# Kernel optimization log

Hardware: AMD Instinct MI355X
Metric: run time of the kernel (lower is better)

## Reference

```python
import jax, jax.numpy as jnp
import numpy as np

B, S, D = 2, 1024, 2048
L = 4
HQ, HKV, HD = 32, 8, 64
I = 5632
V = 32000
EPS = 1e-5
THETA = 10000.0
SCALE = HD ** -0.5
GROUP = HQ // HKV


def setup_inputs() -> dict:
    key = jax.random.key(0)
    ks = jax.random.split(key, 8)
    s = 0.02
    return {
        "input_ids": jax.random.randint(ks[0], (B, S), 0, V, dtype=jnp.int32),
        "positions": jnp.broadcast_to(jnp.arange(S, dtype=jnp.int32), (B, S)),
        "embed": jax.random.normal(ks[1], (V, D), jnp.float32) * s,
        "w_qkv": jax.random.normal(ks[2], (L, D, (HQ + 2 * HKV) * HD), jnp.float32) * s,
        "w_o": jax.random.normal(ks[3], (L, HQ * HD, D), jnp.float32) * s,
        "w_gate_up": jax.random.normal(ks[4], (L, D, 2 * I), jnp.float32) * s,
        "w_down": jax.random.normal(ks[5], (L, I, D), jnp.float32) * s,
        "ln1_w": jnp.ones((L, D), jnp.float32),
        "ln2_w": jnp.ones((L, D), jnp.float32),
        "norm_w": jnp.ones((D,), jnp.float32),
    }


def rmsnorm(x, w):
    var = jnp.mean(x * x, axis=-1, keepdims=True)
    return x * jax.lax.rsqrt(var + EPS) * w


def rope(positions, x):
    # x: [B, S, H, HD]; neox-style rotate-half RoPE
    inv_freq = 1.0 / (THETA ** (jnp.arange(0, HD, 2, dtype=jnp.float32) / HD))
    ang = positions.astype(jnp.float32)[..., None] * inv_freq  # [B, S, HD/2]
    cos = jnp.cos(ang)[:, :, None, :]
    sin = jnp.sin(ang)[:, :, None, :]
    x1, x2 = jnp.split(x, 2, axis=-1)
    return jnp.concatenate([x1 * cos - x2 * sin, x2 * cos + x1 * sin], axis=-1)


def llama_forward(input_ids, positions, embed, w_qkv, w_o, w_gate_up, w_down,
                  ln1_w, ln2_w, norm_w):
    h = embed[input_ids]                      # [B, S, D]
    res = jnp.zeros_like(h)
    causal = jnp.tril(jnp.ones((S, S), dtype=bool))
    neg = jnp.asarray(jnp.finfo(h.dtype).min, h.dtype)

    def layer(carry, params):
        h, res = carry
        wqkv, wo, wgu, wd, l1, l2 = params
        # fused RMSNorm + residual-add (vllm RMSNorm(x, residual) semantics)
        res = h + res
        h = rmsnorm(res, l1)
        # QKV projection + RoPE
        qkv = h @ wqkv
        q, k, v = jnp.split(qkv, [HQ * HD, (HQ + HKV) * HD], axis=-1)
        q = q.reshape(B, S, HQ, HD)
        k = k.reshape(B, S, HKV, HD)
        v = v.reshape(B, S, HKV, HD)
        q = rope(positions, q)
        k = rope(positions, k)
        # GQA: broadcast kv heads across query groups
        k = jnp.repeat(k, GROUP, axis=2)      # [B, S, HQ, HD]
        v = jnp.repeat(v, GROUP, axis=2)
        scores = jnp.einsum('bqhd,bkhd->bhqk', q, k) * SCALE
        scores = jnp.where(causal, scores, neg)
        attn = jax.nn.softmax(scores, axis=-1)
        o = jnp.einsum('bhqk,bkhd->bqhd', attn, v).reshape(B, S, HQ * HD)
        h = o @ wo
        # post-attention fused RMSNorm + residual
        res = h + res
        h = rmsnorm(res, l2)
        # SwiGLU MLP
        gu = h @ wgu
        g, u = jnp.split(gu, 2, axis=-1)
        h = (jax.nn.silu(g) * u) @ wd
        return (h, res), None

    (h, res), _ = jax.lax.scan(layer, (h, res),
                               (w_qkv, w_o, w_gate_up, w_down, ln1_w, ln2_w))
    return rmsnorm(h + res, norm_w)


def reference(input_ids, positions, embed, w_qkv, w_o, w_gate_up, w_down,
              ln1_w, ln2_w, norm_w):
    return llama_forward(input_ids, positions, embed, w_qkv, w_o, w_gate_up,
                         w_down, ln1_w, ln2_w, norm_w)
```

## Files before the change

### kernel.cpp

```cpp
#include <hip/hip_runtime.h>
#include <hip/hip_bf16.h>

#define B_ 2
#define S_ 1024
#define T_ (B_*S_)
#define D_ 2048
#define L_ 4
#define HQ_ 32
#define HKV_ 8
#define HD_ 64
#define I_ 5632
#define EPS_ 1e-5f
#define SCALE_ 0.125f

typedef __attribute__((ext_vector_type(4))) float  float4v;
typedef __attribute__((ext_vector_type(8))) short  short8v;
typedef __attribute__((ext_vector_type(4))) short  short4v;

#define GLOAD16(g, l) \
  __builtin_amdgcn_global_load_lds((const __attribute__((address_space(1))) void*)(g), \
                                   (__attribute__((address_space(3))) void*)(l), 16, 0, 0)

__device__ __forceinline__ short f2bf(float f) {
  union { float f; unsigned u; } c; c.f = f;
  unsigned u = c.u + 0x7fffu + ((c.u >> 16) & 1u);
  return (short)(u >> 16);
}

__device__ __forceinline__ void xcd_swizzle(int gx, int gy, int& bx, int& by) {
  int nwg = gx * gy;
  int orig = by * gx + bx;
  int q = nwg >> 3, r = nwg & 7;
  int xcd = orig & 7, loc = orig >> 3;
  int swz = (xcd < r ? xcd * (q + 1) : r * (q + 1) + (xcd - r) * q) + loc;
  bx = swz / gy;
  by = swz - bx * gy;
}

__global__ __launch_bounds__(256)
void transpose_layer(const float* __restrict__ wq, const float* __restrict__ wo,
                     const float* __restrict__ wg, const float* __restrict__ wd,
                     short* __restrict__ tq, short* __restrict__ to_,
                     short* __restrict__ tg, short* __restrict__ td) {
  int id = blockIdx.x;
  const float* in; short* out; int K, N, bxt, byt;
  if (id < 1536)      { in = wq; out = tq;
                        K = 2048; N = 3072;  bxt = id % 48;  byt = id / 48; }
  else if (id < 2560) { id -= 1536; in = wo; out = to_;
                        K = 2048; N = 2048;  bxt = id % 32;  byt = id / 32; }
  else if (id < 8192) { id -= 2560; in = wg; out = tg;
                        K = 2048; N = 11264; bxt = id % 176; byt = id / 176; }
  else                { id -= 8192; in = wd; out = td;
                        K = 5632; N = 2048;  bxt = id % 32;  byt = id / 32; }
  __shared__ float t[64][65];
  const int bx = bxt * 64;
  const int by = byt * 64;
  const int tid = threadIdx.x;
  const int lr = tid >> 4;
  const int lc = (tid & 15) * 4;
  #pragma unroll
  for (int j = 0; j < 64; j += 16) {
    float4v v = *(const float4v*)(in + (size_t)(by + lr + j) * N + bx + lc);
    t[lr + j][lc] = v[0]; t[lr + j][lc + 1] = v[1];
    t[lr + j][lc + 2] = v[2]; t[lr + j][lc + 3] = v[3];
  }
  __syncthreads();
  const int nr = tid >> 3;
  const int kc = (tid & 7) * 8;
  #pragma unroll
  for (int j = 0; j < 64; j += 32) {
    short8v y;
    #pragma unroll
    for (int e = 0; e < 8; e++) y[e] = f2bf(t[kc + e][nr + j]);
    *(short8v*)(out + (size_t)(bx + nr + j) * K + by + kc) = y;
  }
}

__global__ __launch_bounds__(256)
void embed_gather(const int* __restrict__ ids, const float* __restrict__ embed,
                  float* __restrict__ h) {
  size_t i = (size_t)blockIdx.x * 256 + threadIdx.x;
  int t  = (int)(i >> 9);
  int d4 = (int)(i & 511);
  ((float4v*)h)[i] = ((const float4v*)(embed + (size_t)ids[t] * D_))[d4];
}

__global__ __launch_bounds__(256)
void rmsnorm_kernel(const float* __restrict__ x, float* __restrict__ res,
                    const float* __restrict__ w, void* __restrict__ outp,
                    int first, int bf16out) {
  const int row = blockIdx.x;
  const int tid = threadIdx.x;
  const size_t base = (size_t)row * D_;
  float4v v0, v1;
  if (first) {
    v0 = ((const float4v*)(x + base))[tid * 2];
    v1 = ((const float4v*)(x + base))[tid * 2 + 1];
    ((float4v*)(res + base))[tid * 2]     = v0;
    ((float4v*)(res + base))[tid * 2 + 1] = v1;
  } else {
    v0 = ((const float4v*)(res + base))[tid * 2];
    v1 = ((const float4v*)(res + base))[tid * 2 + 1];
  }
  float ss = v0[0]*v0[0] + v0[1]*v0[1] + v0[2]*v0[2] + v0[3]*v0[3]
           + v1[0]*v1[0] + v1[1]*v1[1] + v1[2]*v1[2] + v1[3]*v1[3];
  #pragma unroll
  for (int off = 32; off > 0; off >>= 1) ss += __shfl_xor(ss, off, 64);
  __shared__ float red[4];
  if ((tid & 63) == 0) red[tid >> 6] = ss;
  __syncthreads();
  float tot = red[0] + red[1] + red[2] + red[3];
  float rs = rsqrtf(tot * (1.0f / D_) + EPS_);
  float4v w0 = ((const float4v*)w)[tid * 2];
  float4v w1 = ((const float4v*)w)[tid * 2 + 1];
  float4v o0 = v0 * rs * w0;
  float4v o1 = v1 * rs * w1;
  if (bf16out) {
    short8v y;
    #pragma unroll
    for (int k = 0; k < 4; k++) { y[k] = f2bf(o0[k]); y[k + 4] = f2bf(o1[k]); }
    ((short8v*)((char*)outp + base * 2))[tid] = y;
  } else {
    float* op = (float*)outp + base;
    ((float4v*)op)[tid * 2]     = o0;
    ((float4v*)op)[tid * 2 + 1] = o1;
  }
}

__global__ __launch_bounds__(512, 4)
void gemm_big128(const short* __restrict__ A, const short* __restrict__ Bt,
                 float* __restrict__ C, int M, int N, int K, int addto) {
  __shared__ short sA[2][128 * 64];
  __shared__ short sB[2][128 * 64];
  int bx = blockIdx.x, by = blockIdx.y;
  xcd_swizzle(gridDim.x, gridDim.y, bx, by);
  const int tid  = threadIdx.x;
  const int lane = tid & 63;
  const int wv   = tid >> 6;
  const int wr   = wv >> 2;
  const int wc   = wv & 3;
  const int row0 = by * 128;
  const int col0 = bx * 128;
  const int fr = lane & 15;
  const int g  = lane >> 4;
  const int NT = K >> 6;

  float4v acc[4][2] = {};

  int rS[2], cS[2];
  #pragma unroll
  for (int k = 0; k < 2; k++) {
    int s = tid + k * 512;
    rS[k] = s >> 3;
    cS[k] = (((s & 7) ^ (rS[k] & 7)) << 3);
  }

#define STAGE128(t, buf) do { \
    int k0_ = (t) << 6; \
    _Pragma("unroll") \
    for (int k_ = 0; k_ < 2; k_++) \
      GLOAD16(A  + (size_t)(row0 + rS[k_]) * K + k0_ + cS[k_], \
              &sA[buf][(tid + k_ * 512) * 8]); \
    _Pragma("unroll") \
    for (int k_ = 0; k_ < 2; k_++) \
      GLOAD16(Bt + (size_t)(col0 + rS[k_]) * K + k0_ + cS[k_], \
              &sB[buf][(tid + k_ * 512) * 8]); \
  } while (0)

  STAGE128(0, 0);

  for (int t = 0; t < NT; t++) {
    const int cur = t & 1;
    if (t + 1 < NT) {
      STAGE128(t + 1, cur ^ 1);
      asm volatile("s_waitcnt vmcnt(4)" ::: "memory");
    } else {
      asm volatile("s_waitcnt vmcnt(0)" ::: "memory");
    }
    __builtin_amdgcn_s_barrier();
    __builtin_amdgcn_sched_barrier(0);

    const short* pA = &sA[cur][(wr * 64) * 64];
    const short* pB = &sB[cur][(wc * 32) * 64];
    #pragma unroll
    for (int ks = 0; ks < 2; ks++) {
      const int fswk = ((((ks << 2) | g) ^ (fr & 7)) << 3);
      short8v bfr[2], afr[4];
      #pragma unroll
      for (int ni = 0; ni < 2; ni++)
        bfr[ni] = *(const short8v*)(pB + (ni * 16 + fr) * 64 + fswk);
      #pragma unroll
      for (int m4 = 0; m4 < 4; m4++)
        afr[m4] = *(const short8v*)(pA + (m4 * 16 + fr) * 64 + fswk);
      __builtin_amdgcn_s_setprio(1);
      #pragma unroll
      for (int m4 = 0; m4 < 4; m4++)
        #pragma unroll
        for (int ni = 0; ni < 2; ni++)
          acc[m4][ni] = __builtin_amdgcn_mfma_f32_16x16x32_bf16(
              afr[m4], bfr[ni], acc[m4][ni], 0, 0, 0);
      __builtin_amdgcn_s_setprio(0);
    }
    asm volatile("" ::: "memory");
    __builtin_amdgcn_s_barrier();
  }

  #pragma unroll
  for (int m4 = 0; m4 < 4; m4++)
    #pragma unroll
    for (int ni = 0; ni < 2; ni++) {
      size_t base = (size_t)(row0 + wr * 64 + m4 * 16 + g * 4) * N
                    + col0 + wc * 32 + ni * 16 + fr;
      if (addto) {
        #pragma unroll
        for (int r = 0; r < 4; r++)
          C[base + (size_t)r * N] += acc[m4][ni][r];
      } else {
        #pragma unroll
        for (int r = 0; r < 4; r++)
          C[base + (size_t)r * N] = acc[m4][ni][r];
      }
    }
#undef STAGE128
}

__global__ __launch_bounds__(512, 2)
void gemm_glu_big(const short* __restrict__ A, const short* __restrict__ Bt,
                  short* __restrict__ mlp, int K) {
  __shared__ short sA[2][128 * 64];
  __shared__ short sG[2][128 * 64];
  __shared__ short sU[2][128 * 64];
  int bx = blockIdx.x, by = blockIdx.y;
  xcd_swizzle(gridDim.x, gridDim.y, bx, by);
  const int tid  = threadIdx.x;
  const int lane = tid & 63;
  const int wv   = tid >> 6;
  const int wr   = wv >> 2;
  const int wc   = wv & 3;
  const int row0 = by * 128;
  const int col0 = bx * 128;
  const int fr = lane & 15;
  const int g  = lane >> 4;
  const int NT = K >> 6;

  float4v accg[4][2] = {};
  float4v accu[4][2] = {};

  int rS[2], cS[2];
  #pragma unroll
  for (int k = 0; k < 2; k++) {
    int s = tid + k * 512;
    rS[k] = s >> 3;
    cS[k] = (((s & 7) ^ (rS[k] & 7)) << 3);
  }

#define STAGEGLU(t, buf) do { \
    int k0_ = (t) << 6; \
    _Pragma("unroll") \
    for (int k_ = 0; k_ < 2; k_++) \
      GLOAD16(A  + (size_t)(row0 + rS[k_]) * K + k0_ + cS[k_], \
              &sA[buf][(tid + k_ * 512) * 8]); \
    _Pragma("unroll") \
    for (int k_ = 0; k_ < 2; k_++) \
      GLOAD16(Bt + (size_t)(col0 + rS[k_]) * K + k0_ + cS[k_], \
              &sG[buf][(tid + k_ * 512) * 8]); \
    _Pragma("unroll") \
    for (int k_ = 0; k_ < 2; k_++) \
      GLOAD16(Bt + (size_t)(col0 + I_ + rS[k_]) * K + k0_ + cS[k_], \
              &sU[buf][(tid + k_ * 512) * 8]); \
  } while (0)

  STAGEGLU(0, 0);

  for (int t = 0; t < NT; t++) {
    const int cur = t & 1;
    if (t + 1 < NT) {
      STAGEGLU(t + 1, cur ^ 1);
      asm volatile("s_waitcnt vmcnt(6)" ::: "memory");
    } else {
      asm volatile("s_waitcnt vmcnt(0)" ::: "memory");
    }
    __builtin_amdgcn_s_barrier();
    __builtin_amdgcn_sched_barrier(0);

    const short* pA = &sA[cur][(wr * 64) * 64];
    const short* pG = &sG[cur][(wc * 32) * 64];
    const short* pU = &sU[cur][(wc * 32) * 64];
    #pragma unroll
    for (int ks = 0; ks < 2; ks++) {
      const int fswk = ((((ks << 2) | g) ^ (fr & 7)) << 3);
      short8v bg[2], bu[2], afr[4];
      #pragma unroll
      for (int ni = 0; ni < 2; ni++) {
        bg[ni] = *(const short8v*)(pG + (ni * 16 + fr) * 64 + fswk);
        bu[ni] = *(const short8v*)(pU + (ni * 16 + fr) * 64 + fswk);
      }
      #pragma unroll
      for (int m4 = 0; m4 < 4; m4++)
        afr[m4] = *(const short8v*)(pA + (m4 * 16 + fr) * 64 + fswk);
      __builtin_amdgcn_s_setprio(1);
      #pragma unroll
      for (int m4 = 0; m4 < 4; m4++)
        #pragma unroll
        for (int ni = 0; ni < 2; ni++) {
          accg[m4][ni] = __builtin_amdgcn_mfma_f32_16x16x32_bf16(
              afr[m4], bg[ni], accg[m4][ni], 0, 0, 0);
          accu[m4][ni] = __builtin_amdgcn_mfma_f32_16x16x32_bf16(
              afr[m4], bu[ni], accu[m4][ni], 0, 0, 0);
        }
      __builtin_amdgcn_s_setprio(0);
    }
    asm volatile("" ::: "memory");
    __builtin_amdgcn_s_barrier();
  }

  #pragma unroll
  for (int m4 = 0; m4 < 4; m4++)
    #pragma unroll
    for (int ni = 0; ni < 2; ni++) {
      size_t base = (size_t)(row0 + wr * 64 + m4 * 16 + g * 4) * I_
                    + col0 + wc * 32 + ni * 16 + fr;
      #pragma unroll
      for (int r = 0; r < 4; r++) {
        float gv = accg[m4][ni][r], uv = accu[m4][ni][r];
        mlp[base + (size_t)r * I_] = f2bf(gv / (1.0f + __expf(-gv)) * uv);
      }
    }
#undef STAGEGLU
}

__global__ __launch_bounds__(512, 4)
void gemm_qkv_big(const short* __restrict__ A, const short* __restrict__ Bt,
                  const float* __restrict__ tab, short* __restrict__ qbf,
                  short* __restrict__ kbf, short* __restrict__ vtbf, int K) {
  __shared__ short sA[2][128 * 64];
  __shared__ short sB[2][128 * 64];
  int bx = blockIdx.x, by = blockIdx.y;
  xcd_swizzle(gridDim.x, gridDim.y, bx, by);
  const int tid  = threadIdx.x;
  const int lane = tid & 63;
  const int wv   = tid >> 6;
  const int wm   = (wv >> 1) * 32;
  const int wn   = (wv & 1) * 64;
  const int row0 = by * 128;
  const int col0 = bx * 128;
  const int fr = lane & 15;
  const int g  = lane >> 4;
  const int NT = K >> 6;

  float4v acc[2][4] = {};

  int rS[2], cS[2];
  #pragma unroll
  for (int k = 0; k < 2; k++) {
    int s = tid + k * 512;
    rS[k] = s >> 3;
    cS[k] = (((s & 7) ^ (rS[k] & 7)) << 3);
  }

#define STAGEQKV(t, buf) do { \
    int k0_ = (t) << 6; \
    _Pragma("unroll") \
    for (int k_ = 0; k_ < 2; k_++) \
      GLOAD16(A  + (size_t)(row0 + rS[k_]) * K + k0_ + cS[k_], \
              &sA[buf][(tid + k_ * 512) * 8]); \
    _Pragma("unroll") \
    for (int k_ = 0; k_ < 2; k_++) \
      GLOAD16(Bt + (size_t)(col0 + rS[k_]) * K + k0_ + cS[k_], \
              &sB[buf][(tid + k_ * 512) * 8]); \
  } while (0)

  STAGEQKV(0, 0);

  for (int t = 0; t < NT; t++) {
    const int cur = t & 1;
    if (t + 1 < NT) {
      STAGEQKV(t + 1, cur ^ 1);
      asm volatile("s_waitcnt vmcnt(4)" ::: "memory");
    } else {
      asm volatile("s_waitcnt vmcnt(0)" ::: "memory");
    }
    __builtin_amdgcn_s_barrier();
    __builtin_amdgcn_sched_barrier(0);

    const short* pA = &sA[cur][wm * 64];
    const short* pB = &sB[cur][wn * 64];
    #pragma unroll
    for (int ks = 0; ks < 2; ks++) {
      const int fswk = ((((ks << 2) | g) ^ (fr & 7)) << 3);
      short8v afr[2], bfr[4];
      #pragma unroll
      for (int m2 = 0; m2 < 2; m2++)
        afr[m2] = *(const short8v*)(pA + (m2 * 16 + fr) * 64 + fswk);
      #pragma unroll
      for (int ni = 0; ni < 4; ni++)
        bfr[ni] = *(const short8v*)(pB + (ni * 16 + fr) * 64 + fswk);
      __builtin_amdgcn_s_setprio(1);
      #pragma unroll
      for (int m2 = 0; m2 < 2; m2++)
        #pragma unroll
        for (int ni = 0; ni < 4; ni++)
          acc[m2][ni] = __builtin_amdgcn_mfma_f32_16x16x32_bf16(
              afr[m2], bfr[ni], acc[m2][ni], 0, 0, 0);
      __builtin_amdgcn_s_setprio(0);
    }
    asm volatile("" ::: "memory");
    __builtin_amdgcn_s_barrier();
  }

  const int head = (col0 + wn) >> 6;
  if (head < HQ_ + HKV_) {
    const float sc = (head < HQ_) ? SCALE_ : 1.0f;
    short* dst = (head < HQ_) ? qbf : kbf;
    const int hh = (head < HQ_) ? head : head - HQ_;
    const int HN = (head < HQ_) ? HQ_ : HKV_;
    #pragma unroll
    for (int m2 = 0; m2 < 2; m2++)
      #pragma unroll
      for (int jj = 0; jj < 2; jj++)
        #pragma unroll
        for (int r = 0; r < 4; r++) {
          int m = row0 + wm + m2 * 16 + g * 4 + r;
          int b = m >> 10, s = m & (S_ - 1);
          int d1 = jj * 16 + fr;
          float x1 = acc[m2][jj][r], x2 = acc[m2][jj + 2][r];
          const float* tb = tab + (size_t)m * 64 + d1 * 2;
          float c = tb[0], sn = tb[1];
          size_t base = ((size_t)((b * HN + hh) * S_ + s)) * HD_;
          dst[base + d1]      = f2bf((x1 * c - x2 * sn) * sc);
          dst[base + d1 + 32] = f2bf((x2 * c + x1 * sn) * sc);
        }
  } else {
    const int vh = head - HQ_ - HKV_;
    #pragma unroll
    for (int m2 = 0; m2 < 2; m2++) {
      int m0 = row0 + wm + m2 * 16 + g * 4;
      int b = m0 >> 10, s0 = m0 & (S_ - 1);
      #pragma unroll
      for (int ni = 0; ni < 4; ni++) {
        int d = ni * 16 + fr;
        short4v w;
        #pragma unroll
        for (int r = 0; r < 4; r++) w[r] = f2bf(acc[m2][ni][r]);
        *(short4v*)(&vtbf[((size_t)((b * HKV_ + vh) * HD_ + d)) * S_ + s0]) = w;
      }
    }
  }
#undef STAGEQKV
}

__global__ __launch_bounds__(256)
void rope_table(const int* __restrict__ pos, float* __restrict__ tab) {
  int i = blockIdx.x * 256 + threadIdx.x;
  int t = i >> 5, ii = i & 31;
  float p = (float)pos[t];
  float freq = __expf(-(float)ii * (9.210340371976184f / 32.0f));
  float ang = p * freq;
  tab[2 * i]     = cosf(ang);
  tab[2 * i + 1] = sinf(ang);
}

#define KPAD 68

__global__ __launch_bounds__(512)
void attn_mfma(const short* __restrict__ qbf, const short* __restrict__ kbf,
               const short* __restrict__ vtbf, short* __restrict__ obf) {
  __shared__ short sK[64 * KPAD];
  __shared__ short sVt[64 * KPAD];
  __shared__ short sP[8][16 * KPAD];
  const int qb = blockIdx.x;
  const int h  = blockIdx.y;
  const int b  = blockIdx.z;
  const int kh = h >> 2;
  const int tid  = threadIdx.x;
  const int lane = tid & 63;
  const int wv   = tid >> 6;
  const int q0 = qb * 128;
  const int cc = lane & 15;
  const int g  = lane >> 4;

  short8v qf0, qf1;
  {
    const short* qrow = qbf + ((size_t)((b * HQ_ + h) * S_ + q0 + wv * 16 + cc)) * HD_;
    qf0 = *(const short8v*)(qrow + g * 8);
    qf1 = *(const short8v*)(qrow + g * 8 + 32);
  }
  float4v accO[4] = {};
  float m_r[4], l_r[4];
  #pragma unroll
  for (int r = 0; r < 4; r++) { m_r[r] = -1e30f; l_r[r] = 0.f; }

  const short* kb = kbf  + ((size_t)(b * HKV_ + kh)) * S_ * HD_;
  const short* vb = vtbf + ((size_t)(b * HKV_ + kh)) * HD_ * S_;

  const int rr = tid >> 3;
  const int ch = (tid & 7) * 8;

  short8v kr = *(const short8v*)(kb + (size_t)rr * HD_ + ch);
  short8v vr = *(const short8v*)(vb + (size_t)rr * S_ + ch);

  const int nb = 2 * qb + 1;
  for (int jt = 0; jt <= nb; jt++) {
    const int j0 = jt * 64;
    __syncthreads();
    *(short8v*)(&sK[rr * KPAD + ch])  = kr;
    *(short8v*)(&sVt[rr * KPAD + ch]) = vr;
    __syncthreads();

    if (jt < nb) {
      const int j0n = j0 + 64;
      kr = *(const short8v*)(kb + (size_t)(j0n + rr) * HD_ + ch);
      vr = *(const short8v*)(vb + (size_t)rr * S_ + j0n + ch);
    }

    float4v sc[4] = {};
    #pragma unroll
    for (int ct = 0; ct < 4; ct++) {
      short8v k0 = *(const short8v*)(&sK[(ct * 16 + cc) * KPAD + g * 8]);
      short8v k1 = *(const short8v*)(&sK[(ct * 16 + cc) * KPAD + g * 8 + 32]);
      __builtin_amdgcn_s_setprio(1);
      sc[ct] = __builtin_amdgcn_mfma_f32_16x16x32_bf16(qf0, k0, sc[ct], 0, 0, 0);
      sc[ct] = __builtin_amdgcn_mfma_f32_16x16x32_bf16(qf1, k1, sc[ct], 0, 0, 0);
      __builtin_amdgcn_s_setprio(0);
    }
    if (jt >= 2 * qb) {
      #pragma unroll
      for (int ct = 0; ct < 4; ct++)
        #pragma unroll
        for (int r = 0; r < 4; r++)
          if (j0 + ct * 16 + cc > q0 + wv * 16 + g * 4 + r) sc[ct][r] = -1e30f;
    }
    float pmv[4], dmax = -1e30f;
    #pragma unroll
    for (int r = 0; r < 4; r++) {
      float pm = fmaxf(fmaxf(sc[0][r], sc[1][r]), fmaxf(sc[2][r], sc[3][r]));
      pm = fmaxf(pm, __shfl_xor(pm, 1, 64));
      pm = fmaxf(pm, __shfl_xor(pm, 2, 64));
      pm = fmaxf(pm, __shfl_xor(pm, 4, 64));
      pm = fmaxf(pm, __shfl_xor(pm, 8, 64));
      pmv[r] = pm;
      dmax = fmaxf(dmax, pm - m_r[r]);
    }
    if (!__all(dmax <= 8.0f)) {
      float corr[4];
      #pragma unroll
      for (int r = 0; r < 4; r++) {
        float mn = fmaxf(m_r[r], pmv[r]);
        corr[r] = __expf(m_r[r] - mn);
        m_r[r] = mn;
        l_r[r] *= corr[r];
      }
      #pragma unroll
      for (int dt = 0; dt < 4; dt++)
        #pragma unroll
        for (int r = 0; r < 4; r++)
          accO[dt][r] *= corr[r];
    }
    #pragma unroll
    for (int r = 0; r < 4; r++) {
      float rs = 0.f;
      #pragma unroll
      for (int ct = 0; ct < 4; ct++) {
        float p = __expf(sc[ct][r] - m_r[r]);
        sc[ct][r] = p;
        rs += p;
      }
      rs += __shfl_xor(rs, 1, 64);
      rs += __shfl_xor(rs, 2, 64);
      rs += __shfl_xor(rs, 4, 64);
      rs += __shfl_xor(rs, 8, 64);
      l_r[r] += rs;
    }
    #pragma unroll
    for (int ct = 0; ct < 4; ct++)
      #pragma unroll
      for (int r = 0; r < 4; r++)
        sP[wv][(g * 4 + r) * KPAD + ct * 16 + cc] = f2bf(sc[ct][r]);
    short8v pf0 = *(const short8v*)(&sP[wv][cc * KPAD + g * 8]);
    short8v pf1 = *(const short8v*)(&sP[wv][cc * KPAD + g * 8 + 32]);
    #pragma unroll
    for (int dt = 0; dt < 4; dt++) {
      short8v v0 = *(const short8v*)(&sVt[(dt * 16 + cc) * KPAD + g * 8]);
      short8v v1 = *(const short8v*)(&sVt[(dt * 16 + cc) * KPAD + g * 8 + 32]);
      __builtin_amdgcn_s_setprio(1);
      accO[dt] = __builtin_amdgcn_mfma_f32_16x16x32_bf16(pf0, v0, accO[dt], 0, 0, 0);
      accO[dt] = __builtin_amdgcn_mfma_f32_16x16x32_bf16(pf1, v1, accO[dt], 0, 0, 0);
      __builtin_amdgcn_s_setprio(0);
    }
  }
  #pragma unroll
  for (int dt = 0; dt < 4; dt++)
    #pragma unroll
    for (int r = 0; r < 4; r++) {
      int q = q0 + wv * 16 + g * 4 + r;
      obf[((size_t)(b * S_ + q)) * 2048 + h * 64 + dt * 16 + cc] = f2bf(accO[dt][r] / l_r[r]);
    }
}

extern "C" void kernel_launch(void* const* d_in, const int* in_sizes, int n_in,
                              void* d_out, int out_size, void* d_ws, size_t ws_size,
                              hipStream_t stream) {
  const int*   ids   = (const int*)d_in[0];
  const int*   pos   = (const int*)d_in[1];
  const float* embed = (const float*)d_in[2];
  const float* w_qkv = (const float*)d_in[3];
  const float* w_o   = (const float*)d_in[4];
  const float* w_gu  = (const float*)d_in[5];
  const float* w_dn  = (const float*)d_in[6];
  const float* ln1   = (const float*)d_in[7];
  const float* ln2   = (const float*)d_in[8];
  const float* normw = (const float*)d_in[9];
  float* out = (float*)d_out;

  char* p = (char*)d_ws;
  short* wTq  = (short*)p; p += (size_t)2048 * 3072 * 2;
  short* wTo  = (short*)p; p += (size_t)2048 * 2048 * 2;
  short* wTgu = (short*)p; p += (size_t)2048 * 11264 * 2;
  short* wTdn = (short*)p; p += (size_t)5632 * 2048 * 2;
  float* h     = (float*)p; p += (size_t)T_ * D_ * 4;
  float* res   = (float*)p; p += (size_t)T_ * D_ * 4;
  short* hnbf  = (short*)p; p += (size_t)T_ * D_ * 2;
  short* obf   = (short*)p; p += (size_t)T_ * D_ * 2;
  short* mlpbf = (short*)p; p += (size_t)T_ * I_ * 2;
  float* tab   = (float*)p; p += (size_t)T_ * 64 * 4;
  short* qbf   = (short*)p; p += (size_t)B_ * HQ_ * S_ * HD_ * 2;
  short* kbf   = (short*)p; p += (size_t)B_ * HKV_ * S_ * HD_ * 2;
  short* vtbf  = (short*)p; p += (size_t)B_ * HKV_ * HD_ * S_ * 2;

  embed_gather<<<T_ * D_ / 4 / 256, 256, 0, stream>>>(ids, embed, h);
  rope_table<<<T_ * 32 / 256, 256, 0, stream>>>(pos, tab);

  for (int l = 0; l < L_; l++) {
    transpose_layer<<<11008, 256, 0, stream>>>(
        w_qkv + (size_t)l * 2048 * 3072, w_o + (size_t)l * 2048 * 2048,
        w_gu + (size_t)l * 2048 * 11264, w_dn + (size_t)l * 5632 * 2048,
        wTq, wTo, wTgu, wTdn);

    rmsnorm_kernel<<<T_, 256, 0, stream>>>(h, res, ln1 + l * D_, hnbf,
                                           l == 0 ? 1 : 0, 1);

    gemm_qkv_big<<<dim3(3072 / 128, T_ / 128), 512, 0, stream>>>(
        hnbf, wTq, tab, qbf, kbf, vtbf, 2048);

    attn_mfma<<<dim3(8, 32, 2), 512, 0, stream>>>(qbf, kbf, vtbf, obf);

    gemm_big128<<<dim3(2048 / 128, T_ / 128), 512, 0, stream>>>(
        obf, wTo, res, T_, 2048, 2048, 1);

    rmsnorm_kernel<<<T_, 256, 0, stream>>>(nullptr, res, ln2 + l * D_, hnbf, 0, 1);

    gemm_glu_big<<<dim3(I_ / 128, T_ / 128), 512, 0, stream>>>(
        hnbf, wTgu, mlpbf, 2048);

    gemm_big128<<<dim3(2048 / 128, T_ / 128), 512, 0, stream>>>(
        mlpbf, wTdn, res, T_, 2048, 5632, 1);
  }
  rmsnorm_kernel<<<T_, 256, 0, stream>>>(nullptr, res, normw, out, 0, 0);
}
```

Before: 1.679 ms.

## Register-based weight transpose and LDS-free attention with smaller causal tiles

The weight transpose kernel drops its shared-memory tile. Each thread now loads eight rows of float4 into registers and writes short8 bf16 columns directly, which halves the block count and removes the barrier. The attention kernel stops staging K and V^T through LDS with block-wide barriers. Each wave reads its MFMA operands straight from global/L2, and blocks shrink to 64 query rows and 256 threads so causal work is finer-grained. This trades LDS reuse for more redundant global loads and uncoalesced 16-byte transposed writes.

Result: slower. 1.999 ms (+19.0%).

```diff
diff --git a/kernel.cpp b/kernel.cpp
--- a/kernel.cpp
+++ b/kernel.cpp
@@ -44,35 +44,29 @@
                      short* __restrict__ tg, short* __restrict__ td) {
   int id = blockIdx.x;
   const float* in; short* out; int K, N, bxt, byt;
-  if (id < 1536)      { in = wq; out = tq;
-                        K = 2048; N = 3072;  bxt = id % 48;  byt = id / 48; }
-  else if (id < 2560) { id -= 1536; in = wo; out = to_;
-                        K = 2048; N = 2048;  bxt = id % 32;  byt = id / 32; }
-  else if (id < 8192) { id -= 2560; in = wg; out = tg;
-                        K = 2048; N = 11264; bxt = id % 176; byt = id / 176; }
-  else                { id -= 8192; in = wd; out = td;
-                        K = 5632; N = 2048;  bxt = id % 32;  byt = id / 32; }
-  __shared__ float t[64][65];
-  const int bx = bxt * 64;
-  const int by = byt * 64;
-  const int tid = threadIdx.x;
-  const int lr = tid >> 4;
-  const int lc = (tid & 15) * 4;
-  #pragma unroll
-  for (int j = 0; j < 64; j += 16) {
-    float4v v = *(const float4v*)(in + (size_t)(by + lr + j) * N + bx + lc);
-    t[lr + j][lc] = v[0]; t[lr + j][lc + 1] = v[1];
-    t[lr + j][lc + 2] = v[2]; t[lr + j][lc + 3] = v[3];
-  }
-  __syncthreads();
-  const int nr = tid >> 3;
-  const int kc = (tid & 7) * 8;
-  #pragma unroll
-  for (int j = 0; j < 64; j += 32) {
+  if (id < 768)       { in = wq; out = tq;
+                        K = 2048; N = 3072;  bxt = id % 12; byt = id / 12; }
+  else if (id < 1280) { id -= 768;  in = wo; out = to_;
+                        K = 2048; N = 2048;  bxt = id % 8;  byt = id / 8; }
+  else if (id < 4096) { id -= 1280; in = wg; out = tg;
+                        K = 2048; N = 11264; bxt = id % 44; byt = id / 44; }
+  else                { id -= 4096; in = wd; out = td;
+                        K = 5632; N = 2048;  bxt = id % 8;  byt = id / 8; }
+  const int tid  = threadIdx.x;
+  const int lane = tid & 63;
+  const int wv   = tid >> 6;
+  const int n0 = bxt * 256 + lane * 4;
+  const int k0 = byt * 32 + wv * 8;
+  float4v v[8];
+  #pragma unroll
+  for (int e = 0; e < 8; e++)
+    v[e] = *(const float4v*)(in + (size_t)(k0 + e) * N + n0);
+  #pragma unroll
+  for (int i = 0; i < 4; i++) {
     short8v y;
     #pragma unroll
-    for (int e = 0; e < 8; e++) y[e] = f2bf(t[kc + e][nr + j]);
-    *(short8v*)(out + (size_t)(bx + nr + j) * K + by + kc) = y;
+    for (int e = 0; e < 8; e++) y[e] = f2bf(v[e][i]);
+    *(short8v*)(out + (size_t)(n0 + i) * K + k0) = y;
   }
 }
 
@@ -462,26 +456,24 @@
 
 #define KPAD 68
 
-__global__ __launch_bounds__(512)
+__global__ __launch_bounds__(256)
 void attn_mfma(const short* __restrict__ qbf, const short* __restrict__ kbf,
                const short* __restrict__ vtbf, short* __restrict__ obf) {
-  __shared__ short sK[64 * KPAD];
-  __shared__ short sVt[64 * KPAD];
-  __shared__ short sP[8][16 * KPAD];
-  const int qb = blockIdx.x;
+  __shared__ short sP[4][16 * KPAD];
+  const int qblk = blockIdx.x;
   const int h  = blockIdx.y;
   const int b  = blockIdx.z;
   const int kh = h >> 2;
   const int tid  = threadIdx.x;
   const int lane = tid & 63;
   const int wv   = tid >> 6;
-  const int q0 = qb * 128;
+  const int q0 = qblk * 64 + wv * 16;
   const int cc = lane & 15;
   const int g  = lane >> 4;
 
   short8v qf0, qf1;
   {
-    const short* qrow = qbf + ((size_t)((b * HQ_ + h) * S_ + q0 + wv * 16 + cc)) * HD_;
+    const short* qrow = qbf + ((size_t)((b * HQ_ + h) * S_ + q0 + cc)) * HD_;
     qf0 = *(const short8v*)(qrow + g * 8);
     qf1 = *(const short8v*)(qrow + g * 8 + 32);
   }
@@ -493,42 +485,25 @@
   const short* kb = kbf  + ((size_t)(b * HKV_ + kh)) * S_ * HD_;
   const short* vb = vtbf + ((size_t)(b * HKV_ + kh)) * HD_ * S_;
 
-  const int rr = tid >> 3;
-  const int ch = (tid & 7) * 8;
-
-  short8v kr = *(const short8v*)(kb + (size_t)rr * HD_ + ch);
-  short8v vr = *(const short8v*)(vb + (size_t)rr * S_ + ch);
-
-  const int nb = 2 * qb + 1;
-  for (int jt = 0; jt <= nb; jt++) {
+  for (int jt = 0; jt <= qblk; jt++) {
     const int j0 = jt * 64;
-    __syncthreads();
-    *(short8v*)(&sK[rr * KPAD + ch])  = kr;
-    *(short8v*)(&sVt[rr * KPAD + ch]) = vr;
-    __syncthreads();
-
-    if (jt < nb) {
-      const int j0n = j0 + 64;
-      kr = *(const short8v*)(kb + (size_t)(j0n + rr) * HD_ + ch);
-      vr = *(const short8v*)(vb + (size_t)rr * S_ + j0n + ch);
-    }
-
     float4v sc[4] = {};
     #pragma unroll
     for (int ct = 0; ct < 4; ct++) {
-      short8v k0 = *(const short8v*)(&sK[(ct * 16 + cc) * KPAD + g * 8]);
-      short8v k1 = *(const short8v*)(&sK[(ct * 16 + cc) * KPAD + g * 8 + 32]);
+      const short* kr = kb + (size_t)(j0 + ct * 16 + cc) * HD_ + g * 8;
+      short8v k0 = *(const short8v*)kr;
+      short8v k1 = *(const short8v*)(kr + 32);
       __builtin_amdgcn_s_setprio(1);
       sc[ct] = __builtin_amdgcn_mfma_f32_16x16x32_bf16(qf0, k0, sc[ct], 0, 0, 0);
       sc[ct] = __builtin_amdgcn_mfma_f32_16x16x32_bf16(qf1, k1, sc[ct], 0, 0, 0);
       __builtin_amdgcn_s_setprio(0);
     }
-    if (jt >= 2 * qb) {
+    if (jt == qblk) {
       #pragma unroll
       for (int ct = 0; ct < 4; ct++)
         #pragma unroll
         for (int r = 0; r < 4; r++)
-          if (j0 + ct * 16 + cc > q0 + wv * 16 + g * 4 + r) sc[ct][r] = -1e30f;
+          if (j0 + ct * 16 + cc > q0 + g * 4 + r) sc[ct][r] = -1e30f;
     }
     float pmv[4], dmax = -1e30f;
     #pragma unroll
@@ -580,8 +555,9 @@
     short8v pf1 = *(const short8v*)(&sP[wv][cc * KPAD + g * 8 + 32]);
     #pragma unroll
     for (int dt = 0; dt < 4; dt++) {
-      short8v v0 = *(const short8v*)(&sVt[(dt * 16 + cc) * KPAD + g * 8]);
-      short8v v1 = *(const short8v*)(&sVt[(dt * 16 + cc) * KPAD + g * 8 + 32]);
+      const short* vr = vb + (size_t)(dt * 16 + cc) * S_ + j0 + g * 8;
+      short8v v0 = *(const short8v*)vr;
+      short8v v1 = *(const short8v*)(vr + 32);
       __builtin_amdgcn_s_setprio(1);
       accO[dt] = __builtin_amdgcn_mfma_f32_16x16x32_bf16(pf0, v0, accO[dt], 0, 0, 0);
       accO[dt] = __builtin_amdgcn_mfma_f32_16x16x32_bf16(pf1, v1, accO[dt], 0, 0, 0);
@@ -592,7 +568,7 @@
   for (int dt = 0; dt < 4; dt++)
     #pragma unroll
     for (int r = 0; r < 4; r++) {
-      int q = q0 + wv * 16 + g * 4 + r;
+      int q = q0 + g * 4 + r;
       obf[((size_t)(b * S_ + q)) * 2048 + h * 64 + dt * 16 + cc] = f2bf(accO[dt][r] / l_r[r]);
     }
 }
@@ -631,7 +607,7 @@
   rope_table<<<T_ * 32 / 256, 256, 0, stream>>>(pos, tab);
 
   for (int l = 0; l < L_; l++) {
-    transpose_layer<<<11008, 256, 0, stream>>>(
+    transpose_layer<<<5504, 256, 0, stream>>>(
         w_qkv + (size_t)l * 2048 * 3072, w_o + (size_t)l * 2048 * 2048,
         w_gu + (size_t)l * 2048 * 11264, w_dn + (size_t)l * 5632 * 2048,
         wTq, wTo, wTgu, wTdn);
@@ -642,7 +618,7 @@
     gemm_qkv_big<<<dim3(3072 / 128, T_ / 128), 512, 0, stream>>>(
         hnbf, wTq, tab, qbf, kbf, vtbf, 2048);
 
-    attn_mfma<<<dim3(8, 32, 2), 512, 0, stream>>>(qbf, kbf, vtbf, obf);
+    attn_mfma<<<dim3(16, 32, 2), 256, 0, stream>>>(qbf, kbf, vtbf, obf);
 
     gemm_big128<<<dim3(2048 / 128, T_ / 128), 512, 0, stream>>>(
         obf, wTo, res, T_, 2048, 2048, 1);
```

## Overlap next layer's weight transpose with GLU GEMM via extra blocks

Applied to the files above, without the earlier changes.

Weight transposition for layer l+1 now runs as extra workgroups appended to the GLU GEMM launch of layer l, writing into a double-buffered set of bf16 weight buffers. Only layer 0 is transposed in a standalone launch. This aims to fill idle CUs during the GLU GEMM and remove the serialized per-layer transpose launches. In exchange it doubles the workspace for transposed weights, and the transpose blocks share the GEMM kernel's 96KB LDS footprint and launch bounds, which may lower their occupancy.

New measurement: 1.700 ms. Within noise of the previous version (+1.3%).

```diff
diff --git a/kernel.cpp b/kernel.cpp
--- a/kernel.cpp
+++ b/kernel.cpp
@@ -37,13 +37,34 @@
   by = swz - bx * gy;
 }
 
-__global__ __launch_bounds__(256)
-void transpose_layer(const float* __restrict__ wq, const float* __restrict__ wo,
-                     const float* __restrict__ wg, const float* __restrict__ wd,
-                     short* __restrict__ tq, short* __restrict__ to_,
-                     short* __restrict__ tg, short* __restrict__ td) {
-  int id = blockIdx.x;
-  const float* in; short* out; int K, N, bxt, byt;
+__device__ __forceinline__ void tr_tile(const float* __restrict__ in,
+                                        short* __restrict__ out, int K, int N,
+                                        int bx, int by, int tid,
+                                        float (*t)[65]) {
+  const int lr = tid >> 4;
+  const int lc = (tid & 15) * 4;
+  #pragma unroll
+  for (int j = 0; j < 64; j += 16) {
+    float4v v = *(const float4v*)(in + (size_t)(by + lr + j) * N + bx + lc);
+    t[lr + j][lc] = v[0]; t[lr + j][lc + 1] = v[1];
+    t[lr + j][lc + 2] = v[2]; t[lr + j][lc + 3] = v[3];
+  }
+  __syncthreads();
+  const int nr = tid >> 3;
+  const int kc = (tid & 7) * 8;
+  #pragma unroll
+  for (int j = 0; j < 64; j += 32) {
+    short8v y;
+    #pragma unroll
+    for (int e = 0; e < 8; e++) y[e] = f2bf(t[kc + e][nr + j]);
+    *(short8v*)(out + (size_t)(bx + nr + j) * K + by + kc) = y;
+  }
+}
+
+__device__ __forceinline__ void tr_decode(int id,
+    const float* wq, const float* wo, const float* wg, const float* wd,
+    short* tq, short* to_, short* tg, short* td,
+    const float*& in, short*& out, int& K, int& N, int& bxt, int& byt) {
   if (id < 1536)      { in = wq; out = tq;
                         K = 2048; N = 3072;  bxt = id % 48;  byt = id / 48; }
   else if (id < 2560) { id -= 1536; in = wo; out = to_;
@@ -52,28 +73,17 @@
                         K = 2048; N = 11264; bxt = id % 176; byt = id / 176; }
   else                { id -= 8192; in = wd; out = td;
                         K = 5632; N = 2048;  bxt = id % 32;  byt = id / 32; }
+}
+
+__global__ __launch_bounds__(256)
+void transpose_layer(const float* __restrict__ wq, const float* __restrict__ wo,
+                     const float* __restrict__ wg, const float* __restrict__ wd,
+                     short* __restrict__ tq, short* __restrict__ to_,
+                     short* __restrict__ tg, short* __restrict__ td) {
   __shared__ float t[64][65];
-  const int bx = bxt * 64;
-  const int by = byt * 64;
-  const int tid = threadIdx.x;
-  const int lr = tid >> 4;
-  const int lc = (tid & 15) * 4;
-  #pragma unroll
-  for (int j = 0; j < 64; j += 16) {
-    float4v v = *(const float4v*)(in + (size_t)(by + lr + j) * N + bx + lc);
-    t[lr + j][lc] = v[0]; t[lr + j][lc + 1] = v[1];
-    t[lr + j][lc + 2] = v[2]; t[lr + j][lc + 3] = v[3];
-  }
-  __syncthreads();
-  const int nr = tid >> 3;
-  const int kc = (tid & 7) * 8;
-  #pragma unroll
-  for (int j = 0; j < 64; j += 32) {
-    short8v y;
-    #pragma unroll
-    for (int e = 0; e < 8; e++) y[e] = f2bf(t[kc + e][nr + j]);
-    *(short8v*)(out + (size_t)(bx + nr + j) * K + by + kc) = y;
-  }
+  const float* in; short* out; int K, N, bxt, byt;
+  tr_decode(blockIdx.x, wq, wo, wg, wd, tq, to_, tg, td, in, out, K, N, bxt, byt);
+  tr_tile(in, out, K, N, bxt * 64, byt * 64, threadIdx.x, t);
 }
 
 __global__ __launch_bounds__(256)
@@ -224,14 +234,34 @@
 #undef STAGE128
 }
 
+#define GLU_BLKS 704
 __global__ __launch_bounds__(512, 2)
-void gemm_glu_big(const short* __restrict__ A, const short* __restrict__ Bt,
-                  short* __restrict__ mlp, int K) {
-  __shared__ short sA[2][128 * 64];
-  __shared__ short sG[2][128 * 64];
-  __shared__ short sU[2][128 * 64];
-  int bx = blockIdx.x, by = blockIdx.y;
-  xcd_swizzle(gridDim.x, gridDim.y, bx, by);
+void gemm_glu_tr(const short* __restrict__ A, const short* __restrict__ Bt,
+                 short* __restrict__ mlp, int K,
+                 const float* __restrict__ nwq, const float* __restrict__ nwo,
+                 const float* __restrict__ nwg, const float* __restrict__ nwd,
+                 short* __restrict__ ntq, short* __restrict__ nto,
+                 short* __restrict__ ntg, short* __restrict__ ntd) {
+  __shared__ __align__(16) char smem[98304];
+  short* sAb = (short*)smem;
+  short* sGb = (short*)(smem + 32768);
+  short* sUb = (short*)(smem + 65536);
+  const int flat = blockIdx.x;
+
+  if (flat >= GLU_BLKS) {
+    const int half = threadIdx.x >> 8;
+    const int tid2 = threadIdx.x & 255;
+    int tile = (flat - GLU_BLKS) * 2 + half;
+    const float* in; short* out; int Kt, Nt, bxt, byt;
+    tr_decode(tile, nwq, nwo, nwg, nwd, ntq, nto, ntg, ntd,
+              in, out, Kt, Nt, bxt, byt);
+    float (*t)[65] = (float(*)[65])(smem + half * 16640);
+    tr_tile(in, out, Kt, Nt, bxt * 64, byt * 64, tid2, t);
+    return;
+  }
+
+  int bx = flat % 44, by = flat / 44;
+  xcd_swizzle(44, 16, bx, by);
   const int tid  = threadIdx.x;
   const int lane = tid & 63;
   const int wv   = tid >> 6;
@@ -259,15 +289,15 @@
     _Pragma("unroll") \
     for (int k_ = 0; k_ < 2; k_++) \
       GLOAD16(A  + (size_t)(row0 + rS[k_]) * K + k0_ + cS[k_], \
-              &sA[buf][(tid + k_ * 512) * 8]); \
+              sAb + (buf) * 8192 + (tid + k_ * 512) * 8); \
     _Pragma("unroll") \
     for (int k_ = 0; k_ < 2; k_++) \
       GLOAD16(Bt + (size_t)(col0 + rS[k_]) * K + k0_ + cS[k_], \
-              &sG[buf][(tid + k_ * 512) * 8]); \
+              sGb + (buf) * 8192 + (tid + k_ * 512) * 8); \
     _Pragma("unroll") \
     for (int k_ = 0; k_ < 2; k_++) \
       GLOAD16(Bt + (size_t)(col0 + I_ + rS[k_]) * K + k0_ + cS[k_], \
-              &sU[buf][(tid + k_ * 512) * 8]); \
+              sUb + (buf) * 8192 + (tid + k_ * 512) * 8); \
   } while (0)
 
   STAGEGLU(0, 0);
@@ -283,9 +313,9 @@
     __builtin_amdgcn_s_barrier();
     __builtin_amdgcn_sched_barrier(0);
 
-    const short* pA = &sA[cur][(wr * 64) * 64];
-    const short* pG = &sG[cur][(wc * 32) * 64];
-    const short* pU = &sU[cur][(wc * 32) * 64];
+    const short* pA = sAb + cur * 8192 + (wr * 64) * 64;
+    const short* pG = sGb + cur * 8192 + (wc * 32) * 64;
+    const short* pU = sUb + cur * 8192 + (wc * 32) * 64;
     #pragma unroll
     for (int ks = 0; ks < 2; ks++) {
       const int fswk = ((((ks << 2) | g) ^ (fr & 7)) << 3);
@@ -613,10 +643,13 @@
   float* out = (float*)d_out;
 
   char* p = (char*)d_ws;
-  short* wTq  = (short*)p; p += (size_t)2048 * 3072 * 2;
-  short* wTo  = (short*)p; p += (size_t)2048 * 2048 * 2;
-  short* wTgu = (short*)p; p += (size_t)2048 * 11264 * 2;
-  short* wTdn = (short*)p; p += (size_t)5632 * 2048 * 2;
+  short* wTq[2];  short* wTo[2];  short* wTgu[2];  short* wTdn[2];
+  for (int s = 0; s < 2; s++) {
+    wTq[s]  = (short*)p; p += (size_t)2048 * 3072 * 2;
+    wTo[s]  = (short*)p; p += (size_t)2048 * 2048 * 2;
+    wTgu[s] = (short*)p; p += (size_t)2048 * 11264 * 2;
+    wTdn[s] = (short*)p; p += (size_t)5632 * 2048 * 2;
+  }
   float* h     = (float*)p; p += (size_t)T_ * D_ * 4;
   float* res   = (float*)p; p += (size_t)T_ * D_ * 4;
   short* hnbf  = (short*)p; p += (size_t)T_ * D_ * 2;
@@ -630,30 +663,36 @@
   embed_gather<<<T_ * D_ / 4 / 256, 256, 0, stream>>>(ids, embed, h);
   rope_table<<<T_ * 32 / 256, 256, 0, stream>>>(pos, tab);
 
+  transpose_layer<<<11008, 256, 0, stream>>>(
+      w_qkv, w_o, w_gu, w_dn, wTq[0], wTo[0], wTgu[0], wTdn[0]);
+
   for (int l = 0; l < L_; l++) {
-    transpose_layer<<<11008, 256, 0, stream>>>(
-        w_qkv + (size_t)l * 2048 * 3072, w_o + (size_t)l * 2048 * 2048,
-        w_gu + (size_t)l * 2048 * 11264, w_dn + (size_t)l * 5632 * 2048,
-        wTq, wTo, wTgu, wTdn);
+    const int cs = l & 1;
+    const int ns = (l + 1) & 1;
+    const int ln = (l < L_ - 1) ? l + 1 : 0;
 
     rmsnorm_kernel<<<T_, 256, 0, stream>>>(h, res, ln1 + l * D_, hnbf,
                                            l == 0 ? 1 : 0, 1);
 
     gemm_qkv_big<<<dim3(3072 / 128, T_ / 128), 512, 0, stream>>>(
-        hnbf, wTq, tab, qbf, kbf, vtbf, 2048);
+        hnbf, wTq[cs], tab, qbf, kbf, vtbf, 2048);
 
     attn_mfma<<<dim3(8, 32, 2), 512, 0, stream>>>(qbf, kbf, vtbf, obf);
 
     gemm_big128<<<dim3(2048 / 128, T_ / 128), 512, 0, stream>>>(
-        obf, wTo, res, T_, 2048, 2048, 1);
+        obf, wTo[cs], res, T_, 2048, 2048, 1);
 
     rmsnorm_kernel<<<T_, 256, 0, stream>>>(nullptr, res, ln2 + l * D_, hnbf, 0, 1);
 
-    gemm_glu_big<<<dim3(I_ / 128, T_ / 128), 512, 0, stream>>>(
-        hnbf, wTgu, mlpbf, 2048);
+    const int nblk = (l < L_ - 1) ? (GLU_BLKS + 5504) : GLU_BLKS;
+    gemm_glu_tr<<<nblk, 512, 0, stream>>>(
+        hnbf, wTgu[cs], mlpbf, 2048,
+        w_qkv + (size_t)ln * 2048 * 3072, w_o + (size_t)ln * 2048 * 2048,
+        w_gu + (size_t)ln * 2048 * 11264, w_dn + (size_t)ln * 5632 * 2048,
+        wTq[ns], wTo[ns], wTgu[ns], wTdn[ns]);
 
     gemm_big128<<<dim3(2048 / 128, T_ / 128), 512, 0, stream>>>(
-        mlpbf, wTdn, res, T_, 2048, 5632, 1);
+        mlpbf, wTdn[cs], res, T_, 2048, 5632, 1);
   }
   rmsnorm_kernel<<<T_, 256, 0, stream>>>(nullptr, res, normw, out, 0, 0);
 }
```
